# Optimization experiments

Measured on AMD Instinct MI355X. Metric: run time of the kernel, lower is better.

Reference implementation:

```python
import jax, jax.numpy as jnp
import numpy as np

V, D, H, HA = 10000, 1024, 1024, 128  # ntoken, ninp, nhid, adapt hidden
T, B = 128, 64


def setup_inputs() -> dict:
    key = jax.random.key(0)
    ks = jax.random.split(key, 8)
    u = lambda k, sh, r: jax.random.uniform(k, sh, jnp.float32, -r, r)
    return {
        "tokens": jax.random.randint(ks[0], (T, B), 0, V, dtype=jnp.int32),
        "emb": u(ks[1], (V, D), 0.1),                 # encoder weight, uniform(-0.1,0.1)
        "Wax": u(ks[2], (D, HA), 1.0 / np.sqrt(D)),   # adapt_module input weight
        "Wah": u(ks[3], (HA, HA), 1.0 / np.sqrt(HA)), # adapt_module recurrent weight
        "bah": jnp.zeros((HA,), jnp.float32),
        "Wa": u(ks[4], (HA, 2), 1.0 / np.sqrt(HA)),   # readout -> (n, s)
        "ba": jnp.zeros((2,), jnp.float32),
        "Wih": u(ks[5], (D, H), 1.0 / np.sqrt(D)),    # gamma_rnn input weight
        "Whh": u(ks[6], (H, H), 1.0 / np.sqrt(H)),    # gamma_rnn recurrent weight
        "bh": jnp.zeros((H,), jnp.float32),
        "Wd": u(ks[7], (H, V), 0.1),                  # decoder weight, uniform(-0.1,0.1)
        "bd": jnp.zeros((V,), jnp.float32),           # decoder bias, zeros
    }


def reference(tokens, emb, Wax, Wah, bah, Wa, ba, Wih, Whh, bh, Wd, bd):
    x = emb[tokens]  # [T, B, D] embedding lookup (encoder)
    Bsz = tokens.shape[1]

    def step(carry, x_t):
        h0, h1 = carry
        # adapt_module: small RNN producing per-sample gates a = [n, s]
        h0n = jnp.tanh(x_t @ Wax + h0 @ Wah + bah)            # [B, HA]
        a = jax.nn.sigmoid(h0n @ Wa + ba)                      # [B, 2]
        n, s = a[:, 0:1], a[:, 1:2]
        # gamma_rnn: adaptive-activation vanilla RNN cell
        pre = x_t @ Wih + h1 @ Whh + bh                        # [B, H]
        h1n = (1.0 - s) * jnp.tanh(n * pre) + s * jax.nn.sigmoid(n * pre)
        return (h0n, h1n), h1n

    h0_0 = jnp.zeros((Bsz, HA), x.dtype)
    h1_0 = jnp.zeros((Bsz, H), x.dtype)
    (_, h1_final), hs = jax.lax.scan(step, (h0_0, h1_0), x)   # hs: [T, B, H]
    decoded = hs @ Wd + bd                                     # [T, B, V]
    return decoded, h1_final
```

## Files before the change

kernel.cpp:

```cpp
#include <hip/hip_runtime.h>
#include <hip/hip_bf16.h>
#include <cstdint>
#include <cstddef>

#define TSTEPS 128
#define BATCH  64
#define DDIM   1024
#define HDIM   1024
#define HADIM  128
#define VOCAB  10000
#define MROWS  (TSTEPS * BATCH)
#define NBLK   32

typedef __attribute__((ext_vector_type(8))) short bf16x8;
typedef __attribute__((ext_vector_type(4))) float f32x4;

__device__ __forceinline__ unsigned short f2bf(float x) {
    unsigned int u = __float_as_uint(x);
    unsigned int r = (u + 0x7fffu + ((u >> 16) & 1u)) >> 16;
    return (unsigned short)r;
}

__global__ __launch_bounds__(256) void transpose_cast(const float* __restrict__ W,
                                                      unsigned short* __restrict__ Wt,
                                                      int R, int C) {
    __shared__ float tile[32][33];
    int tc = blockIdx.x * 32;
    int tr = blockIdx.y * 32;
    int tid = threadIdx.x;
    for (int i = 0; i < 4; i++) {
        int idx = tid + i * 256;
        int r = idx >> 5, c = idx & 31;
        float v = 0.f;
        if (tr + r < R && tc + c < C) v = W[(size_t)(tr + r) * C + tc + c];
        tile[r][c] = v;
    }
    __syncthreads();
    for (int i = 0; i < 4; i++) {
        int idx = tid + i * 256;
        int r = idx >> 5, c = idx & 31;
        if (tc + r < C && tr + c < R)
            Wt[(size_t)(tc + r) * R + tr + c] = f2bf(tile[c][r]);
    }
}

__global__ __launch_bounds__(256) void gather_cast(const int* __restrict__ tok,
                                                   const float* __restrict__ emb,
                                                   unsigned short* __restrict__ xb) {
    int i = blockIdx.x;
    int t = tok[i];
    const float4* src = (const float4*)(emb + (size_t)t * DDIM);
    float4 v = src[threadIdx.x];
    ushort4 o;
    o.x = f2bf(v.x); o.y = f2bf(v.y); o.z = f2bf(v.z); o.w = f2bf(v.w);
    ((ushort4*)(xb + (size_t)i * DDIM))[threadIdx.x] = o;
}

__global__ __launch_bounds__(256) void gemm_bt_bias(const unsigned short* __restrict__ A,
                                                    const unsigned short* __restrict__ Bt,
                                                    const float* __restrict__ bias,
                                                    float* __restrict__ C,
                                                    int M, int N, int K) {
    __shared__ unsigned short As[64 * 40];
    __shared__ unsigned short Bs[64 * 40];
    int rowBase = blockIdx.y * 64;
    int colBase = blockIdx.x * 64;
    int tid = threadIdx.x;
    int wave = tid >> 6, lane = tid & 63;
    int wr = wave >> 1, wc = wave & 1;
    int quad = lane >> 4, lr = lane & 15;
    int ldRow = tid >> 2;
    int ldK = (tid & 3) * 8;
    bool bvalid = (colBase + ldRow) < N;
    const unsigned short* Ag = A + (size_t)(rowBase + ldRow) * K + ldK;
    const unsigned short* Bg = Bt + (size_t)(colBase + ldRow) * K + ldK;

    f32x4 acc[2][2] = {};
    for (int k0 = 0; k0 < K; k0 += 32) {
        uint4 av = *(const uint4*)(Ag + k0);
        uint4 bv = {};
        if (bvalid) bv = *(const uint4*)(Bg + k0);
        __syncthreads();
        *(uint4*)(As + ldRow * 40 + ldK) = av;
        *(uint4*)(Bs + ldRow * 40 + ldK) = bv;
        __syncthreads();
        bf16x8 a0 = *(const bf16x8*)(As + (wr * 32 + lr) * 40 + quad * 8);
        bf16x8 a1 = *(const bf16x8*)(As + (wr * 32 + 16 + lr) * 40 + quad * 8);
        bf16x8 b0 = *(const bf16x8*)(Bs + (wc * 32 + lr) * 40 + quad * 8);
        bf16x8 b1 = *(const bf16x8*)(Bs + (wc * 32 + 16 + lr) * 40 + quad * 8);
        acc[0][0] = __builtin_amdgcn_mfma_f32_16x16x32_bf16(a0, b0, acc[0][0], 0, 0, 0);
        acc[0][1] = __builtin_amdgcn_mfma_f32_16x16x32_bf16(a0, b1, acc[0][1], 0, 0, 0);
        acc[1][0] = __builtin_amdgcn_mfma_f32_16x16x32_bf16(a1, b0, acc[1][0], 0, 0, 0);
        acc[1][1] = __builtin_amdgcn_mfma_f32_16x16x32_bf16(a1, b1, acc[1][1], 0, 0, 0);
    }
    for (int mi = 0; mi < 2; mi++)
        for (int ni = 0; ni < 2; ni++) {
            int col = colBase + wc * 32 + ni * 16 + lr;
            if (col < N) {
                float b = bias[col];
                for (int r = 0; r < 4; r++) {
                    int row = rowBase + wr * 32 + mi * 16 + quad * 4 + r;
                    C[(size_t)row * N + col] = acc[mi][ni][r] + b;
                }
            }
        }
}

__global__ __launch_bounds__(128) void h0_chain(const float* __restrict__ Xa,
                                                const float* __restrict__ Wah,
                                                const float* __restrict__ Wa,
                                                const float* __restrict__ ba,
                                                float2* __restrict__ ns) {
    int b = blockIdx.x;
    int j = threadIdx.x;
    __shared__ float WahS[HADIM * HADIM];
    __shared__ float h0s[HADIM];
    __shared__ float red[4];
    for (int i = j; i < HADIM * HADIM; i += 128) WahS[i] = Wah[i];
    h0s[j] = 0.f;
    float wa0 = Wa[j * 2 + 0], wa1 = Wa[j * 2 + 1];
    float ba0 = ba[0], ba1 = ba[1];
    __syncthreads();
    for (int t = 0; t < TSTEPS; t++) {
        float acc = Xa[((size_t)t * BATCH + b) * HADIM + j];
        for (int k = 0; k < HADIM; k++) acc += h0s[k] * WahS[k * HADIM + j];
        float h0n = tanhf(acc);
        float p0 = h0n * wa0, p1 = h0n * wa1;
        for (int off = 32; off > 0; off >>= 1) {
            p0 += __shfl_down(p0, off);
            p1 += __shfl_down(p1, off);
        }
        int wv = j >> 6;
        if ((j & 63) == 0) { red[wv * 2 + 0] = p0; red[wv * 2 + 1] = p1; }
        __syncthreads();
        float n = 1.f / (1.f + __expf(-(red[0] + red[2] + ba0)));
        float s = 1.f / (1.f + __expf(-(red[1] + red[3] + ba1)));
        if (j == 0) ns[t * BATCH + b] = make_float2(n, s);
        h0s[j] = h0n;
        __syncthreads();
    }
}

__global__ __launch_bounds__(512, 2) void rnn_fused(
        const unsigned short* __restrict__ WhhT,
        const float* __restrict__ Xi,
        const float2* __restrict__ ns,
        unsigned short* __restrict__ hs,
        float* __restrict__ h1f,
        unsigned int* __restrict__ bar) {
    __shared__ unsigned short Ws[32 * HDIM];
    const int cgid = blockIdx.x;
    const int tid  = threadIdx.x;
    const int wave = tid >> 6;
    const int lane = tid & 63;
    const int bm   = wave & 3;
    const int nt   = wave >> 2;
    const int quad = lane >> 4, lr = lane & 15;
    const int colBase = cgid * 32;

    for (int i = 0; i < 8; i++) {
        int c   = tid + i * 512;
        int row = c >> 7;
        int cin = c & 127;
        uint4 w = *(const uint4*)(WhhT + (((size_t)(colBase + row)) << 10) + cin * 8);
        int b = (cin * 16) ^ ((row & 7) << 4);
        *(uint4*)((char*)Ws + row * 2048 + b) = w;
    }

    const int batchrow = bm * 16 + lr;
    const int colq = colBase + nt * 16 + quad * 4;
    const int wrow = nt * 16 + lr;
    const char* wbase = (const char*)Ws + wrow * 2048;
    const int rb = (wrow & 7) << 4;

    float4 xi_v = *(const float4*)(Xi + (size_t)batchrow * HDIM + colq);
    float2 g_v  = ns[batchrow];
    __syncthreads();

    for (int t = 0; t < TSTEPS; t++) {
        f32x4 acc[4] = {};
        if (t > 0) {
            const char* hb = (const char*)(hs + ((size_t)(t - 1) * BATCH + batchrow) * HDIM)
                             + quad * 16;
            uint4 hv[32];
            #pragma unroll
            for (int i = 0; i < 32; i++) hv[i] = *(const uint4*)(hb + i * 64);
            #pragma unroll
            for (int kc = 0; kc < 32; kc++) {
                bf16x8 wf = *(const bf16x8*)(wbase + ((kc * 64 + quad * 16) ^ rb));
                acc[kc & 3] = __builtin_amdgcn_mfma_f32_16x16x32_bf16(
                                  wf, *(const bf16x8*)&hv[kc], acc[kc & 3], 0, 0, 0);
            }
        }
        f32x4 a = (acc[0] + acc[1]) + (acc[2] + acc[3]);
        float h1n[4];
        #pragma unroll
        for (int r = 0; r < 4; r++) {
            float pre = a[r] + ((const float*)&xi_v)[r];
            float z  = g_v.x * pre;
            float th = tanhf(z);
            float sg = 1.f / (1.f + __expf(-z));
            h1n[r] = (1.f - g_v.y) * th + g_v.y * sg;
        }
        unsigned long long pk =
              (unsigned long long)f2bf(h1n[0])
            | ((unsigned long long)f2bf(h1n[1]) << 16)
            | ((unsigned long long)f2bf(h1n[2]) << 32)
            | ((unsigned long long)f2bf(h1n[3]) << 48);
        __hip_atomic_store((unsigned long long*)(hs + ((size_t)t * BATCH + batchrow) * HDIM + colq),
                           pk, __ATOMIC_RELAXED, __HIP_MEMORY_SCOPE_AGENT);
        if (t == TSTEPS - 1) {
            *(float4*)(h1f + (size_t)batchrow * HDIM + colq) =
                make_float4(h1n[0], h1n[1], h1n[2], h1n[3]);
        } else {
            xi_v = *(const float4*)(Xi + ((size_t)(t + 1) * BATCH + batchrow) * HDIM + colq);
            g_v  = ns[(t + 1) * BATCH + batchrow];
            asm volatile("s_waitcnt vmcnt(0)" ::: "memory");
            __syncthreads();
            if (tid == 0) {
                __hip_atomic_fetch_add(bar, 1u, __ATOMIC_RELAXED, __HIP_MEMORY_SCOPE_AGENT);
                unsigned need = (unsigned)(t + 1) * NBLK;
                while (__hip_atomic_load(bar, __ATOMIC_RELAXED, __HIP_MEMORY_SCOPE_AGENT) < need) {}
            }
            __syncthreads();
        }
    }
}

extern "C" void kernel_launch(void* const* d_in, const int* in_sizes, int n_in,
                              void* d_out, int out_size, void* d_ws, size_t ws_size,
                              hipStream_t stream) {
    const int*   tokens = (const int*)d_in[0];
    const float* emb    = (const float*)d_in[1];
    const float* Wax    = (const float*)d_in[2];
    const float* Wah    = (const float*)d_in[3];
    const float* bah    = (const float*)d_in[4];
    const float* Wa     = (const float*)d_in[5];
    const float* ba     = (const float*)d_in[6];
    const float* Wih    = (const float*)d_in[7];
    const float* Whh    = (const float*)d_in[8];
    const float* bh     = (const float*)d_in[9];
    const float* Wd     = (const float*)d_in[10];
    const float* bd     = (const float*)d_in[11];
    float* out = (float*)d_out;

    char* ws = (char*)d_ws;
    size_t off = 0;
    auto alloc = [&](size_t bytes) -> void* {
        void* p = ws + off;
        off += (bytes + 255) & ~(size_t)255;
        return p;
    };
    unsigned short* WihT = (unsigned short*)alloc((size_t)HDIM * DDIM * 2);
    unsigned short* WaxT = (unsigned short*)alloc((size_t)HADIM * DDIM * 2);
    unsigned short* WhhT = (unsigned short*)alloc((size_t)HDIM * HDIM * 2);
    unsigned short* WdT  = (unsigned short*)alloc((size_t)VOCAB * HDIM * 2);
    unsigned short* xb   = (unsigned short*)alloc((size_t)MROWS * DDIM * 2);
    float*          Xi   = (float*)alloc((size_t)MROWS * HDIM * 4);
    float*          Xa   = (float*)alloc((size_t)MROWS * HADIM * 4);
    unsigned short* hs   = (unsigned short*)alloc((size_t)MROWS * HDIM * 2);
    float2*         ns   = (float2*)alloc((size_t)TSTEPS * BATCH * 8);
    unsigned int*   bar  = (unsigned int*)alloc(256);

    transpose_cast<<<dim3(32, 32), 256, 0, stream>>>(Wih, WihT, DDIM, HDIM);
    transpose_cast<<<dim3(4, 32), 256, 0, stream>>>(Wax, WaxT, DDIM, HADIM);
    transpose_cast<<<dim3(32, 32), 256, 0, stream>>>(Whh, WhhT, HDIM, HDIM);
    transpose_cast<<<dim3(313, 32), 256, 0, stream>>>(Wd, WdT, HDIM, VOCAB);
    gather_cast<<<MROWS, 256, 0, stream>>>(tokens, emb, xb);
    gemm_bt_bias<<<dim3(HDIM / 64, MROWS / 64), 256, 0, stream>>>(xb, WihT, bh, Xi, MROWS, HDIM, DDIM);
    gemm_bt_bias<<<dim3(HADIM / 64, MROWS / 64), 256, 0, stream>>>(xb, WaxT, bah, Xa, MROWS, HADIM, DDIM);
    h0_chain<<<BATCH, 128, 0, stream>>>(Xa, Wah, Wa, ba, ns);
    hipMemsetAsync(bar, 0, sizeof(unsigned int), stream);
    {
        float* h1fin = out + (size_t)MROWS * VOCAB;
        const unsigned short* WhhT_a = WhhT;
        const float*  Xi_a = Xi;
        const float2* ns_a = ns;
        unsigned short* hs_a = hs;
        unsigned int* bar_a = bar;
        void* args[] = { (void*)&WhhT_a, (void*)&Xi_a, (void*)&ns_a, (void*)&hs_a,
                         (void*)&h1fin, (void*)&bar_a };
        hipLaunchCooperativeKernel((const void*)rnn_fused, dim3(NBLK), dim3(512), args, 0, stream);
    }
    gemm_bt_bias<<<dim3((VOCAB + 63) / 64, MROWS / 64), 256, 0, stream>>>(hs, WdT, bd, out, MROWS, VOCAB, HDIM);
}
```

Measured before the change: 2.424 ms.

## Split recurrent RNN over 64 blocks with K-split and per-block flag barrier

The persistent recurrent kernel now runs on 64 cooperative blocks, each owning 16 hidden columns instead of 32. Within a block, the K dimension is split across two wave groups whose partial results are reduced through LDS. The weight tile uses a new conflict-free LDS layout. The single atomic-counter grid barrier is replaced by per-block step flags that wave 0 polls with a wave-wide vote and s_sleep, aiming to cut per-step latency and contention. In exchange each step adds an extra LDS reduction and __syncthreads, and the Xi/ns loads are no longer prefetched a step ahead.

Result: faster. 2.203 ms (-9.1%).

```diff
diff --git a/kernel.cpp b/kernel.cpp
--- a/kernel.cpp
+++ b/kernel.cpp
@@ -10,7 +10,7 @@
 #define HADIM  128
 #define VOCAB  10000
 #define MROWS  (TSTEPS * BATCH)
-#define NBLK   32
+#define CBLK   64
 
 typedef __attribute__((ext_vector_type(8))) short bf16x8;
 typedef __attribute__((ext_vector_type(4))) float f32x4;
@@ -147,80 +147,92 @@
         const float2* __restrict__ ns,
         unsigned short* __restrict__ hs,
         float* __restrict__ h1f,
-        unsigned int* __restrict__ bar) {
-    __shared__ unsigned short Ws[32 * HDIM];
+        unsigned int* __restrict__ flags) {
+    __shared__ unsigned short Ws[16 * HDIM];
+    __shared__ __align__(16) float red[4 * 64 * 4];
     const int cgid = blockIdx.x;
     const int tid  = threadIdx.x;
     const int wave = tid >> 6;
     const int lane = tid & 63;
+    const int kh   = wave >> 2;
     const int bm   = wave & 3;
-    const int nt   = wave >> 2;
     const int quad = lane >> 4, lr = lane & 15;
-    const int colBase = cgid * 32;
-
-    for (int i = 0; i < 8; i++) {
+    const int colBase = cgid * 16;
+
+    for (int i = 0; i < 4; i++) {
         int c   = tid + i * 512;
         int row = c >> 7;
         int cin = c & 127;
         uint4 w = *(const uint4*)(WhhT + (((size_t)(colBase + row)) << 10) + cin * 8);
-        int b = (cin * 16) ^ ((row & 7) << 4);
-        *(uint4*)((char*)Ws + row * 2048 + b) = w;
+        *(uint4*)((char*)Ws + (((cin >> 2) * 64 + (cin & 3) * 16 + row) << 4)) = w;
     }
 
     const int batchrow = bm * 16 + lr;
-    const int colq = colBase + nt * 16 + quad * 4;
-    const int wrow = nt * 16 + lr;
-    const char* wbase = (const char*)Ws + wrow * 2048;
-    const int rb = (wrow & 7) << 4;
-
-    float4 xi_v = *(const float4*)(Xi + (size_t)batchrow * HDIM + colq);
-    float2 g_v  = ns[batchrow];
+    const int colq = colBase + quad * 4;
     __syncthreads();
 
     for (int t = 0; t < TSTEPS; t++) {
+        float4 xi_v = {};
+        float2 g_v  = {};
+        if (kh == 0) {
+            xi_v = *(const float4*)(Xi + ((size_t)t * BATCH + batchrow) * HDIM + colq);
+            g_v  = ns[t * BATCH + batchrow];
+        }
         f32x4 acc[4] = {};
         if (t > 0) {
-            const char* hb = (const char*)(hs + ((size_t)(t - 1) * BATCH + batchrow) * HDIM)
-                             + quad * 16;
-            uint4 hv[32];
+            const unsigned short* hbase = hs + ((size_t)(t - 1) * BATCH + batchrow) * HDIM
+                                          + kh * 512 + quad * 8;
+            uint4 hv[16];
             #pragma unroll
-            for (int i = 0; i < 32; i++) hv[i] = *(const uint4*)(hb + i * 64);
+            for (int i = 0; i < 16; i++) hv[i] = *(const uint4*)(hbase + i * 32);
+            __builtin_amdgcn_sched_barrier(0);
             #pragma unroll
-            for (int kc = 0; kc < 32; kc++) {
-                bf16x8 wf = *(const bf16x8*)(wbase + ((kc * 64 + quad * 16) ^ rb));
-                acc[kc & 3] = __builtin_amdgcn_mfma_f32_16x16x32_bf16(
-                                  wf, *(const bf16x8*)&hv[kc], acc[kc & 3], 0, 0, 0);
+            for (int j = 0; j < 16; j++) {
+                bf16x8 wf = *(const bf16x8*)((const char*)Ws +
+                                ((((kh * 16 + j) * 64 + quad * 16 + lr)) << 4));
+                acc[j & 3] = __builtin_amdgcn_mfma_f32_16x16x32_bf16(
+                                 wf, *(const bf16x8*)&hv[j], acc[j & 3], 0, 0, 0);
             }
         }
         f32x4 a = (acc[0] + acc[1]) + (acc[2] + acc[3]);
-        float h1n[4];
-        #pragma unroll
-        for (int r = 0; r < 4; r++) {
-            float pre = a[r] + ((const float*)&xi_v)[r];
-            float z  = g_v.x * pre;
-            float th = tanhf(z);
-            float sg = 1.f / (1.f + __expf(-z));
-            h1n[r] = (1.f - g_v.y) * th + g_v.y * sg;
-        }
-        unsigned long long pk =
-              (unsigned long long)f2bf(h1n[0])
-            | ((unsigned long long)f2bf(h1n[1]) << 16)
-            | ((unsigned long long)f2bf(h1n[2]) << 32)
-            | ((unsigned long long)f2bf(h1n[3]) << 48);
-        __hip_atomic_store((unsigned long long*)(hs + ((size_t)t * BATCH + batchrow) * HDIM + colq),
-                           pk, __ATOMIC_RELAXED, __HIP_MEMORY_SCOPE_AGENT);
-        if (t == TSTEPS - 1) {
-            *(float4*)(h1f + (size_t)batchrow * HDIM + colq) =
-                make_float4(h1n[0], h1n[1], h1n[2], h1n[3]);
-        } else {
-            xi_v = *(const float4*)(Xi + ((size_t)(t + 1) * BATCH + batchrow) * HDIM + colq);
-            g_v  = ns[(t + 1) * BATCH + batchrow];
+        if (kh == 1) *(f32x4*)&red[(bm * 64 + lane) * 4] = a;
+        __syncthreads();
+        if (kh == 0) {
+            a += *(const f32x4*)&red[(bm * 64 + lane) * 4];
+            float h1n[4];
+            #pragma unroll
+            for (int r = 0; r < 4; r++) {
+                float pre = a[r] + ((const float*)&xi_v)[r];
+                float z  = g_v.x * pre;
+                float th = tanhf(z);
+                float sg = 1.f / (1.f + __expf(-z));
+                h1n[r] = (1.f - g_v.y) * th + g_v.y * sg;
+            }
+            unsigned long long pk =
+                  (unsigned long long)f2bf(h1n[0])
+                | ((unsigned long long)f2bf(h1n[1]) << 16)
+                | ((unsigned long long)f2bf(h1n[2]) << 32)
+                | ((unsigned long long)f2bf(h1n[3]) << 48);
+            __hip_atomic_store((unsigned long long*)(hs + ((size_t)t * BATCH + batchrow) * HDIM + colq),
+                               pk, __ATOMIC_RELAXED, __HIP_MEMORY_SCOPE_AGENT);
+            if (t == TSTEPS - 1)
+                *(float4*)(h1f + (size_t)batchrow * HDIM + colq) =
+                    make_float4(h1n[0], h1n[1], h1n[2], h1n[3]);
+        }
+        if (t < TSTEPS - 1) {
             asm volatile("s_waitcnt vmcnt(0)" ::: "memory");
             __syncthreads();
-            if (tid == 0) {
-                __hip_atomic_fetch_add(bar, 1u, __ATOMIC_RELAXED, __HIP_MEMORY_SCOPE_AGENT);
-                unsigned need = (unsigned)(t + 1) * NBLK;
-                while (__hip_atomic_load(bar, __ATOMIC_RELAXED, __HIP_MEMORY_SCOPE_AGENT) < need) {}
+            if (wave == 0) {
+                if (lane == 0)
+                    __hip_atomic_store(&flags[cgid], (unsigned)(t + 1),
+                                       __ATOMIC_RELAXED, __HIP_MEMORY_SCOPE_AGENT);
+                unsigned need = (unsigned)(t + 1);
+                while (true) {
+                    unsigned v = __hip_atomic_load(&flags[lane],
+                                                   __ATOMIC_RELAXED, __HIP_MEMORY_SCOPE_AGENT);
+                    if (__all(v >= need)) break;
+                    __builtin_amdgcn_s_sleep(1);
+                }
             }
             __syncthreads();
         }
@@ -260,7 +272,7 @@
     float*          Xa   = (float*)alloc((size_t)MROWS * HADIM * 4);
     unsigned short* hs   = (unsigned short*)alloc((size_t)MROWS * HDIM * 2);
     float2*         ns   = (float2*)alloc((size_t)TSTEPS * BATCH * 8);
-    unsigned int*   bar  = (unsigned int*)alloc(256);
+    unsigned int*   flags= (unsigned int*)alloc(CBLK * sizeof(unsigned int));
 
     transpose_cast<<<dim3(32, 32), 256, 0, stream>>>(Wih, WihT, DDIM, HDIM);
     transpose_cast<<<dim3(4, 32), 256, 0, stream>>>(Wax, WaxT, DDIM, HADIM);
@@ -270,17 +282,17 @@
     gemm_bt_bias<<<dim3(HDIM / 64, MROWS / 64), 256, 0, stream>>>(xb, WihT, bh, Xi, MROWS, HDIM, DDIM);
     gemm_bt_bias<<<dim3(HADIM / 64, MROWS / 64), 256, 0, stream>>>(xb, WaxT, bah, Xa, MROWS, HADIM, DDIM);
     h0_chain<<<BATCH, 128, 0, stream>>>(Xa, Wah, Wa, ba, ns);
-    hipMemsetAsync(bar, 0, sizeof(unsigned int), stream);
+    hipMemsetAsync(flags, 0, CBLK * sizeof(unsigned int), stream);
     {
         float* h1fin = out + (size_t)MROWS * VOCAB;
         const unsigned short* WhhT_a = WhhT;
         const float*  Xi_a = Xi;
         const float2* ns_a = ns;
         unsigned short* hs_a = hs;
-        unsigned int* bar_a = bar;
+        unsigned int* flags_a = flags;
         void* args[] = { (void*)&WhhT_a, (void*)&Xi_a, (void*)&ns_a, (void*)&hs_a,
-                         (void*)&h1fin, (void*)&bar_a };
-        hipLaunchCooperativeKernel((const void*)rnn_fused, dim3(NBLK), dim3(512), args, 0, stream);
+                         (void*)&h1fin, (void*)&flags_a };
+        hipLaunchCooperativeKernel((const void*)rnn_fused, dim3(CBLK), dim3(512), args, 0, stream);
     }
     gemm_bt_bias<<<dim3((VOCAB + 63) / 64, MROWS / 64), 256, 0, stream>>>(hs, WdT, bd, out, MROWS, VOCAB, HDIM);
 }
```
